# Optimization experiments

Measured on AMD Instinct MI355X. Metric: run time of the kernel, lower is better.

Reference implementation:

```python
import jax, jax.numpy as jnp
import numpy as np

B, NR, M, NL = 1, 384, 4, 128
IN_C, MID_C, OUT_C = 384, 32, 128


def setup_inputs() -> dict:
    key = jax.random.key(0)
    ks = jax.random.split(key, 24)
    s = 0.02
    d = {
        'rec_1d': jax.random.normal(ks[0], (B, NR, IN_C), jnp.float32),
        'lig_1d': jax.random.normal(ks[1], (B, M, NL, IN_C), jnp.float32),
        'pw_rep': jax.random.normal(ks[2], (B, NR + NL, NR + NL, OUT_C), jnp.float32),
        'rl1_w': jax.random.normal(ks[3], (MID_C, IN_C), jnp.float32) * s,
        'rl1_b': jax.random.normal(ks[4], (MID_C,), jnp.float32) * s,
        'rl2_w': jax.random.normal(ks[5], (MID_C, IN_C), jnp.float32) * s,
        'rl2_b': jax.random.normal(ks[6], (MID_C,), jnp.float32) * s,
        'll1_w': jax.random.normal(ks[7], (MID_C, IN_C), jnp.float32) * s,
        'll1_b': jax.random.normal(ks[8], (MID_C,), jnp.float32) * s,
        'll2_w': jax.random.normal(ks[9], (MID_C, IN_C), jnp.float32) * s,
        'll2_b': jax.random.normal(ks[10], (MID_C,), jnp.float32) * s,
        'rr_w': jax.random.normal(ks[11], (OUT_C, MID_C * MID_C), jnp.float32) * s,
        'rr_b': jax.random.normal(ks[12], (OUT_C,), jnp.float32) * s,
        'rl_w': jax.random.normal(ks[13], (OUT_C, MID_C * MID_C), jnp.float32) * s,
        'rl_b': jax.random.normal(ks[14], (OUT_C,), jnp.float32) * s,
        'lr_w': jax.random.normal(ks[15], (OUT_C, MID_C * MID_C), jnp.float32) * s,
        'lr_b': jax.random.normal(ks[16], (OUT_C,), jnp.float32) * s,
        'll_w': jax.random.normal(ks[17], (OUT_C, MID_C * MID_C), jnp.float32) * s,
        'll_b': jax.random.normal(ks[18], (OUT_C,), jnp.float32) * s,
    }
    return d


def reference(rec_1d, lig_1d, pw_rep,
              rl1_w, rl1_b, rl2_w, rl2_b,
              ll1_w, ll1_b, ll2_w, ll2_b,
              rr_w, rr_b, rl_w, rl_b, lr_w, lr_b, ll_w, ll_b):
    mid_c = rl1_w.shape[0]
    m = lig_1d.shape[1]

    # 1D projections (nn.Linear: x @ W.T + b)
    r_i = rec_1d @ rl1_w.T + rl1_b          # [b, NR, mid]
    r_j = rec_1d @ rl2_w.T + rl2_b          # [b, NR, mid]
    l_i = lig_1d @ ll1_w.T + ll1_b          # [b, m, NL, mid]
    l_j = lig_1d @ ll2_w.T + ll2_b          # [b, m, NL, mid]

    # final Linear weights over flattened (x, y) -> [out, x, y] (y fastest, matching .view)
    Wrr = rr_w.reshape(-1, mid_c, mid_c)
    Wrl = rl_w.reshape(-1, mid_c, mid_c)
    Wlr = lr_w.reshape(-1, mid_c, mid_c)
    Wll = ll_w.reshape(-1, mid_c, mid_c)

    # rr[b,i,j,o] = sum_xy r_i[b,i,x] r_j[b,j,y] Wrr[o,x,y]
    # contract projection weight with one factor first (OpenFold trick):
    rr = jnp.einsum('bioy,bjy->bijo', jnp.einsum('bix,oxy->bioy', r_i, Wrr), r_j) + rr_b

    # mean over m commutes with the broadcast outer products for rl/lr
    l_j_mean = l_j.mean(axis=1)             # [b, NL, mid]
    l_i_mean = l_i.mean(axis=1)             # [b, NL, mid]

    rl = jnp.einsum('bioy,bjy->bijo', jnp.einsum('bix,oxy->bioy', r_i, Wrl), l_j_mean) + rl_b

    # lr output is [b, j_lig, i_res, o]: x-axis from r_j, y-axis from l_i
    lr = jnp.einsum('bioy,bjy->bjio', jnp.einsum('bix,oxy->bioy', r_j, Wlr), l_i_mean) + lr_b

    # ll: mean over m of per-copy outer products (not separable)
    ll = jnp.einsum('bmioy,bmjy->bijo', jnp.einsum('bmix,oxy->bmioy', l_i, Wll), l_j) / m + ll_b

    top = jnp.concatenate([rr, rl], axis=2)  # [b, NR, NR+NL, out]
    bot = jnp.concatenate([lr, ll], axis=2)  # [b, NL, NR+NL, out]
    pw_update = jnp.concatenate([top, bot], axis=1).astype(pw_rep.dtype)
    return pw_update
```

## Files before the change

kernel.cpp:

```cpp
#include <hip/hip_runtime.h>

#define NRES 384
#define NLIG 128
#define INC 384
#define OUTC 128
#define NTOT 512

#define WS_RI   0
#define WS_RJ   12288
#define WS_LI   24576
#define WS_LJ   40960
#define WS_BF16 57344

#define BT_RR   0
#define BT_RL   1572864
#define BT_LR   3145728
#define BT_LL   4718592
#define BF_RJ   6815744
#define BF_LJM  6828032
#define BF_LIM  6832128
#define BF_LJ   6836224
#define BF_RI   6852608
#define BF_LI   6864896
#define BW_W    6881280

typedef __bf16 bf16x8 __attribute__((ext_vector_type(8)));
typedef __bf16 bf16x4 __attribute__((ext_vector_type(4)));
typedef float  f32x4  __attribute__((ext_vector_type(4)));

__device__ inline bf16x8 cvt8(const float* p) {
  f32x4 a = *(const f32x4*)p, b = *(const f32x4*)(p + 4);
  bf16x8 r;
  r[0] = (__bf16)a[0]; r[1] = (__bf16)a[1]; r[2] = (__bf16)a[2]; r[3] = (__bf16)a[3];
  r[4] = (__bf16)b[0]; r[5] = (__bf16)b[1]; r[6] = (__bf16)b[2]; r[7] = (__bf16)b[3];
  return r;
}

__global__ __launch_bounds__(256) void kP_proj(
    const float* __restrict__ rec, const float* __restrict__ lig,
    const float* __restrict__ rl1w, const float* __restrict__ rl1b,
    const float* __restrict__ rl2w, const float* __restrict__ rl2b,
    const float* __restrict__ ll1w, const float* __restrict__ ll1b,
    const float* __restrict__ ll2w, const float* __restrict__ ll2b,
    const float* __restrict__ Wrr, const float* __restrict__ Wrl,
    const float* __restrict__ Wlr, const float* __restrict__ Wll,
    float* __restrict__ ws) {
  __shared__ float lds[32 * 33];
  int b = blockIdx.x, t = threadIdx.x;
  __bf16* B16 = (__bf16*)(ws + WS_BF16);
  if (b >= 28) {
    int bb = b - 28;
    int tt = bb >> 7, o = bb & 127;
    const float* W = tt == 0 ? Wrr : tt == 1 ? Wrl : tt == 2 ? Wlr : Wll;
    __bf16* Wb = B16 + BW_W + tt * 131072;
#pragma unroll
    for (int k = 0; k < 4; ++k) {
      int idx = k * 256 + t;
      int x = idx >> 5, y = idx & 31;
      lds[y * 33 + x] = W[(size_t)o * 1024 + idx];
    }
    __syncthreads();
#pragma unroll
    for (int k = 0; k < 4; ++k) {
      int idx = k * 256 + t;
      int y = idx >> 5, x = idx & 31;
      Wb[(size_t)(o * 32 + y) * 32 + x] = (__bf16)lds[y * 33 + x];
    }
    return;
  }
  int l = t & 63, w = t >> 6;
  int lr16 = l & 15, lq = l >> 4;
  int pair = w >> 1, rh = w & 1;

  const float* in;
  const float *w1, *b1, *w2, *b2;
  float *o1, *o2;
  __bf16 *bf1, *bf2;
  int row0;
  if (b < 12) {
    row0 = b * 32;
    in = rec; w1 = rl1w; b1 = rl1b; w2 = rl2w; b2 = rl2b;
    o1 = ws + WS_RI; o2 = ws + WS_RJ;
    bf1 = B16 + BF_RI; bf2 = B16 + BF_RJ;
  } else {
    row0 = (b - 12) * 32;
    in = lig; w1 = ll1w; b1 = ll1b; w2 = ll2w; b2 = ll2b;
    o1 = ws + WS_LI; o2 = ws + WS_LJ;
    bf1 = B16 + BF_LI; bf2 = B16 + BF_LJ;
  }
  const float* wsrc = pair ? w2 : w1;
  const float* bsrc = pair ? b2 : b1;
  float* osrc = pair ? o2 : o1;
  __bf16* bdst = pair ? bf2 : bf1;
  int arow = row0 + rh * 16 + lr16;

  f32x4 acc[2];
#pragma unroll
  for (int ci = 0; ci < 2; ++ci) acc[ci] = (f32x4){0.f, 0.f, 0.f, 0.f};
  for (int ks = 0; ks < 12; ++ks) {
    bf16x8 af = cvt8(in + (size_t)arow * INC + ks * 32 + lq * 8);
#pragma unroll
    for (int ci = 0; ci < 2; ++ci) {
      int ch = ci * 16 + lr16;
      bf16x8 bf = cvt8(wsrc + (size_t)ch * INC + ks * 32 + lq * 8);
      acc[ci] = __builtin_amdgcn_mfma_f32_16x16x32_bf16(af, bf, acc[ci], 0, 0, 0);
    }
  }
#pragma unroll
  for (int ci = 0; ci < 2; ++ci) {
    int c = ci * 16 + lr16;
    float bias = bsrc[c];
#pragma unroll
    for (int e = 0; e < 4; ++e) {
      int r = row0 + rh * 16 + 4 * lq + e;
      float v = acc[ci][e] + bias;
      osrc[r * 32 + c] = v;
      bdst[r * 32 + c] = (__bf16)v;
    }
  }
}

#define TSTR 264
__global__ __launch_bounds__(256) void k2_makeA(float* __restrict__ ws) {
  __shared__ __bf16 tile[128 * TSTR];
  int b = blockIdx.x, t = threadIdx.x;
  __bf16* B16 = (__bf16*)(ws + WS_BF16);
  if (b >= 256) {
    const float* lj = ws + WS_LJ;
    const float* li = ws + WS_LI;
    __bf16* dm = B16 + BF_LJM;
    __bf16* di = B16 + BF_LIM;
    for (int k = 0; k < 16; ++k) {
      int idx = k * 256 + t;
      dm[idx] = (__bf16)(0.25f * (lj[idx] + lj[4096 + idx] + lj[8192 + idx] + lj[12288 + idx]));
      di[idx] = (__bf16)(0.25f * (li[idx] + li[4096 + idx] + li[8192 + idx] + li[12288 + idx]));
    }
    return;
  }
  int tt = b >> 6, sub = b & 63;
  int nt = sub >> 2, mq = sub & 3;
  const __bf16* facB;
  __bf16* At;
  int M;
  if (tt == 0)      { facB = B16 + BF_RI; At = B16 + BT_RR; M = 384; }
  else if (tt == 1) { facB = B16 + BF_RI; At = B16 + BT_RL; M = 384; }
  else if (tt == 2) { facB = B16 + BF_RJ; At = B16 + BT_LR; M = 384; }
  else              { facB = B16 + BF_LI; At = B16 + BT_LL; M = 512; }
  const __bf16* Wb = B16 + BW_W + tt * 131072;
  int l = t & 63, w = t >> 6;
  int lr16 = l & 15, lq = l >> 4;
  int nw = w * 64;
  int n0w = nt * 256 + nw;
  int mspan = M >> 2;
  int mtiles = M >> 6;
  int m0 = mq * mspan;

  bf16x8 wv[4];
#pragma unroll
  for (int q = 0; q < 4; ++q)
    wv[q] = *(const bf16x8*)(Wb + (size_t)(n0w + q * 16 + lr16) * 32 + lq * 8);

  for (int mt = 0; mt < mtiles; ++mt) {
    bf16x8 fv = *(const bf16x8*)(facB + (size_t)(m0 + mt * 16 + lr16) * 32 + lq * 8);
    f32x4 acc[4];
#pragma unroll
    for (int q = 0; q < 4; ++q) acc[q] = (f32x4){0.f, 0.f, 0.f, 0.f};
#pragma unroll
    for (int q = 0; q < 4; ++q)
      acc[q] = __builtin_amdgcn_mfma_f32_16x16x32_bf16(wv[q], fv, acc[q], 0, 0, 0);
    int ml = mt * 16 + lr16;
#pragma unroll
    for (int q = 0; q < 4; ++q) {
      bf16x4 v;
#pragma unroll
      for (int e = 0; e < 4; ++e) v[e] = (__bf16)acc[q][e];
      *(bf16x4*)&tile[ml * TSTR + nw + q * 16 + 4 * lq] = v;
    }
  }
  __syncthreads();
  int total8 = mspan * 32;
  for (int idx = t; idx < total8; idx += 256) {
    int m = idx >> 5, nl = (idx & 31) * 8;
    bf16x8 v = *(const bf16x8*)&tile[m * TSTR + nl];
    *(bf16x8*)(At + (size_t)(m0 + m) * 4096 + nt * 256 + nl) = v;
  }
}

__global__ __launch_bounds__(256) void k3_mfma(
    const float* __restrict__ ws, float* __restrict__ out,
    const float* __restrict__ rrb, const float* __restrict__ rlb,
    const float* __restrict__ lrb, const float* __restrict__ llb) {
  const __bf16* B16 = (const __bf16*)(ws + WS_BF16);
  int b = blockIdx.x, t = threadIdx.x;
  int l = t & 63, w = t >> 6;
  int lr16 = l & 15, lq = l >> 4;

  if (b < 1920) {
    const __bf16* At;
    const __bf16* fc;
    const float* bias;
    float* outp;
    size_t jstr;
    if (b < 1152) {
      int i = b / 3, jt = b - 3 * i;
      At = B16 + BT_RR + (size_t)i * 4096;
      fc = B16 + BF_RJ + jt * 4096;
      bias = rrb; outp = out + ((size_t)i * NTOT + jt * 128) * OUTC; jstr = OUTC;
    } else if (b < 1536) {
      int i = b - 1152;
      At = B16 + BT_RL + (size_t)i * 4096;
      fc = B16 + BF_LJM;
      bias = rlb; outp = out + ((size_t)i * NTOT + NRES) * OUTC; jstr = OUTC;
    } else {
      int i = b - 1536;
      At = B16 + BT_LR + (size_t)i * 4096;
      fc = B16 + BF_LIM;
      bias = lrb; outp = out + (size_t)NRES * NTOT * OUTC + (size_t)i * OUTC;
      jstr = (size_t)NTOT * OUTC;
    }
    bf16x8 fj[2];
#pragma unroll
    for (int jj = 0; jj < 2; ++jj)
      fj[jj] = *(const bf16x8*)(fc + (size_t)(w * 32 + jj * 16 + lr16) * 32 + lq * 8);
    f32x4 acc[2][8];
#pragma unroll
    for (int jj = 0; jj < 2; ++jj)
#pragma unroll
      for (int ot = 0; ot < 8; ++ot) acc[jj][ot] = (f32x4){0.f, 0.f, 0.f, 0.f};
#pragma unroll
    for (int oc = 0; oc < 2; ++oc) {
      bf16x8 av[4];
#pragma unroll
      for (int o4 = 0; o4 < 4; ++o4)
        av[o4] = *(const bf16x8*)(At + (size_t)((oc * 4 + o4) * 16 + lr16) * 32 + lq * 8);
#pragma unroll
      for (int jj = 0; jj < 2; ++jj)
#pragma unroll
        for (int o4 = 0; o4 < 4; ++o4)
          acc[jj][oc * 4 + o4] =
              __builtin_amdgcn_mfma_f32_16x16x32_bf16(av[o4], fj[jj], acc[jj][oc * 4 + o4], 0, 0, 0);
    }
#pragma unroll
    for (int jj = 0; jj < 2; ++jj) {
      int j = w * 32 + jj * 16 + lr16;
#pragma unroll
      for (int ot = 0; ot < 8; ++ot) {
        f32x4 b4 = *(const f32x4*)&bias[ot * 16 + 4 * lq];
        f32x4 v = acc[jj][ot] + b4;
        *(f32x4*)&outp[(size_t)j * jstr + ot * 16 + 4 * lq] = v;
      }
    }
  } else {
    int il = b - 1920;
    f32x4 acc[2][8];
#pragma unroll
    for (int jj = 0; jj < 2; ++jj)
#pragma unroll
      for (int ot = 0; ot < 8; ++ot) acc[jj][ot] = (f32x4){0.f, 0.f, 0.f, 0.f};
    for (int m = 0; m < 4; ++m) {
      const __bf16* At = B16 + BT_LL + (size_t)(m * 128 + il) * 4096;
      const __bf16* fc = B16 + BF_LJ + m * 4096;
      bf16x8 fj[2];
#pragma unroll
      for (int jj = 0; jj < 2; ++jj)
        fj[jj] = *(const bf16x8*)(fc + (size_t)(w * 32 + jj * 16 + lr16) * 32 + lq * 8);
#pragma unroll
      for (int oc = 0; oc < 2; ++oc) {
        bf16x8 av[4];
#pragma unroll
        for (int o4 = 0; o4 < 4; ++o4)
          av[o4] = *(const bf16x8*)(At + (size_t)((oc * 4 + o4) * 16 + lr16) * 32 + lq * 8);
#pragma unroll
        for (int jj = 0; jj < 2; ++jj)
#pragma unroll
          for (int o4 = 0; o4 < 4; ++o4)
            acc[jj][oc * 4 + o4] =
                __builtin_amdgcn_mfma_f32_16x16x32_bf16(av[o4], fj[jj], acc[jj][oc * 4 + o4], 0, 0, 0);
      }
    }
    float* outp = out + ((size_t)(NRES + il) * NTOT + NRES) * OUTC;
#pragma unroll
    for (int jj = 0; jj < 2; ++jj) {
      int j = w * 32 + jj * 16 + lr16;
#pragma unroll
      for (int ot = 0; ot < 8; ++ot) {
        f32x4 b4 = *(const f32x4*)&llb[ot * 16 + 4 * lq];
        f32x4 v = 0.25f * acc[jj][ot] + b4;
        *(f32x4*)&outp[(size_t)j * OUTC + ot * 16 + 4 * lq] = v;
      }
    }
  }
}

extern "C" void kernel_launch(void* const* d_in, const int* in_sizes, int n_in,
                              void* d_out, int out_size, void* d_ws, size_t ws_size,
                              hipStream_t stream) {
  const float* rec  = (const float*)d_in[0];
  const float* lig  = (const float*)d_in[1];
  const float* rl1w = (const float*)d_in[3];
  const float* rl1b = (const float*)d_in[4];
  const float* rl2w = (const float*)d_in[5];
  const float* rl2b = (const float*)d_in[6];
  const float* ll1w = (const float*)d_in[7];
  const float* ll1b = (const float*)d_in[8];
  const float* ll2w = (const float*)d_in[9];
  const float* ll2b = (const float*)d_in[10];
  const float* rrw  = (const float*)d_in[11];
  const float* rrb  = (const float*)d_in[12];
  const float* rlw  = (const float*)d_in[13];
  const float* rlb  = (const float*)d_in[14];
  const float* lrw  = (const float*)d_in[15];
  const float* lrb  = (const float*)d_in[16];
  const float* llw  = (const float*)d_in[17];
  const float* llb  = (const float*)d_in[18];
  float* out = (float*)d_out;
  float* ws  = (float*)d_ws;

  hipLaunchKernelGGL(kP_proj, dim3(540), dim3(256), 0, stream,
                     rec, lig, rl1w, rl1b, rl2w, rl2b, ll1w, ll1b, ll2w, ll2b,
                     rrw, rlw, lrw, llw, ws);
  hipLaunchKernelGGL(k2_makeA, dim3(257), dim3(256), 0, stream, ws);
  hipLaunchKernelGGL(k3_mfma, dim3(2048), dim3(256), 0, stream,
                     ws, out, rrb, rlb, lrb, llb);
}
```

Baseline: 50.79 us.

## Fuse projection and A-matrix build into one kernel, compute ligand means in consumer

```diff
diff --git a/kernel.cpp b/kernel.cpp
--- a/kernel.cpp
+++ b/kernel.cpp
@@ -6,23 +6,17 @@
 #define OUTC 128
 #define NTOT 512
 
-#define WS_RI   0
-#define WS_RJ   12288
-#define WS_LI   24576
-#define WS_LJ   40960
-#define WS_BF16 57344
-
 #define BT_RR   0
 #define BT_RL   1572864
 #define BT_LR   3145728
 #define BT_LL   4718592
 #define BF_RJ   6815744
-#define BF_LJM  6828032
-#define BF_LIM  6832128
-#define BF_LJ   6836224
-#define BF_RI   6852608
-#define BF_LI   6864896
-#define BW_W    6881280
+#define BF_LJ   6828032
+#define BF_LI   6844416
+
+#define FSTR 40
+#define WSTR 40
+#define TSTR 264
 
 typedef __bf16 bf16x8 __attribute__((ext_vector_type(8)));
 typedef __bf16 bf16x4 __attribute__((ext_vector_type(4)));
@@ -36,7 +30,7 @@
   return r;
 }
 
-__global__ __launch_bounds__(256) void kP_proj(
+__global__ __launch_bounds__(256) void kA_make(
     const float* __restrict__ rec, const float* __restrict__ lig,
     const float* __restrict__ rl1w, const float* __restrict__ rl1b,
     const float* __restrict__ rl2w, const float* __restrict__ rl2b,
@@ -45,144 +39,115 @@
     const float* __restrict__ Wrr, const float* __restrict__ Wrl,
     const float* __restrict__ Wlr, const float* __restrict__ Wll,
     float* __restrict__ ws) {
-  __shared__ float lds[32 * 33];
+  __shared__ __align__(16) char arena[77824];
+  __bf16* wb    = (__bf16*)arena;
+  __bf16* tileO = (__bf16*)arena;
+  __bf16* facB  = (__bf16*)(arena + 67584);
+  __bf16* B16 = (__bf16*)ws;
   int b = blockIdx.x, t = threadIdx.x;
-  __bf16* B16 = (__bf16*)(ws + WS_BF16);
-  if (b >= 28) {
-    int bb = b - 28;
-    int tt = bb >> 7, o = bb & 127;
-    const float* W = tt == 0 ? Wrr : tt == 1 ? Wrl : tt == 2 ? Wlr : Wll;
-    __bf16* Wb = B16 + BW_W + tt * 131072;
-#pragma unroll
-    for (int k = 0; k < 4; ++k) {
-      int idx = k * 256 + t;
-      int x = idx >> 5, y = idx & 31;
-      lds[y * 33 + x] = W[(size_t)o * 1024 + idx];
-    }
-    __syncthreads();
-#pragma unroll
-    for (int k = 0; k < 4; ++k) {
-      int idx = k * 256 + t;
-      int y = idx >> 5, x = idx & 31;
-      Wb[(size_t)(o * 32 + y) * 32 + x] = (__bf16)lds[y * 33 + x];
-    }
-    return;
-  }
   int l = t & 63, w = t >> 6;
   int lr16 = l & 15, lq = l >> 4;
-  int pair = w >> 1, rh = w & 1;
-
-  const float* in;
-  const float *w1, *b1, *w2, *b2;
-  float *o1, *o2;
-  __bf16 *bf1, *bf2;
-  int row0;
-  if (b < 12) {
-    row0 = b * 32;
-    in = rec; w1 = rl1w; b1 = rl1b; w2 = rl2w; b2 = rl2b;
-    o1 = ws + WS_RI; o2 = ws + WS_RJ;
-    bf1 = B16 + BF_RI; bf2 = B16 + BF_RJ;
+
+  if (b < 256) {
+    int tt = b >> 6, sub = b & 63;
+    int nt = sub >> 2, mq = sub & 3;
+    const float *in, *w1, *b1, *W;
+    __bf16* AtG;
+    int mspan;
+    if (tt == 0)      { in = rec; w1 = rl1w; b1 = rl1b; W = Wrr; AtG = B16 + BT_RR; mspan = 96; }
+    else if (tt == 1) { in = rec; w1 = rl1w; b1 = rl1b; W = Wrl; AtG = B16 + BT_RL; mspan = 96; }
+    else if (tt == 2) { in = rec; w1 = rl2w; b1 = rl2b; W = Wlr; AtG = B16 + BT_LR; mspan = 96; }
+    else              { in = lig; w1 = ll1w; b1 = ll1b; W = Wll; AtG = B16 + BT_LL; mspan = 128; }
+    int m0 = mq * mspan, o0 = nt * 8;
+
+#pragma unroll
+    for (int it = 0; it < 8; ++it) {
+      int idx4 = it * 256 + t;
+      f32x4 v = *(const f32x4*)(W + (size_t)o0 * 1024 + idx4 * 4);
+      int flat = idx4 * 4;
+      int oo = flat >> 10, r = flat & 1023, x = r >> 5, y0 = r & 31;
+#pragma unroll
+      for (int e = 0; e < 4; ++e)
+        wb[(oo * 32 + y0 + e) * WSTR + x] = (__bf16)v[e];
+    }
+    __syncthreads();
+
+    bf16x8 wv[4];
+    int nw = w * 64;
+#pragma unroll
+    for (int q = 0; q < 4; ++q)
+      wv[q] = *(const bf16x8*)&wb[(nw + q * 16 + lr16) * WSTR + lq * 8];
+
+    int rtiles = mspan >> 4;
+    int tpw = (rtiles * 2) >> 2;
+    for (int ti = 0; ti < tpw; ++ti) {
+      int tile = w * tpw + ti;
+      int rt = tile >> 1, ct = tile & 1;
+      int ch = ct * 16 + lr16;
+      int arow = m0 + rt * 16 + lr16;
+      f32x4 acc = (f32x4){0.f, 0.f, 0.f, 0.f};
+      for (int ks = 0; ks < 12; ++ks) {
+        bf16x8 af = cvt8(in + (size_t)arow * INC + ks * 32 + lq * 8);
+        bf16x8 bf = cvt8(w1 + (size_t)ch * INC + ks * 32 + lq * 8);
+        acc = __builtin_amdgcn_mfma_f32_16x16x32_bf16(af, bf, acc, 0, 0, 0);
+      }
+      float bias = b1[ch];
+#pragma unroll
+      for (int e = 0; e < 4; ++e)
+        facB[(rt * 16 + 4 * lq + e) * FSTR + ch] = (__bf16)(acc[e] + bias);
+    }
+    __syncthreads();
+
+    for (int mt = 0; mt < rtiles; ++mt) {
+      bf16x8 fv = *(const bf16x8*)&facB[(mt * 16 + lr16) * FSTR + lq * 8];
+      f32x4 acc[4];
+#pragma unroll
+      for (int q = 0; q < 4; ++q) acc[q] = (f32x4){0.f, 0.f, 0.f, 0.f};
+#pragma unroll
+      for (int q = 0; q < 4; ++q)
+        acc[q] = __builtin_amdgcn_mfma_f32_16x16x32_bf16(wv[q], fv, acc[q], 0, 0, 0);
+      int ml = mt * 16 + lr16;
+#pragma unroll
+      for (int q = 0; q < 4; ++q) {
+        bf16x4 v;
+#pragma unroll
+        for (int e = 0; e < 4; ++e) v[e] = (__bf16)acc[q][e];
+        *(bf16x4*)&tileO[ml * TSTR + nw + q * 16 + 4 * lq] = v;
+      }
+    }
+    __syncthreads();
+    int total8 = mspan * 32;
+    for (int idx = t; idx < total8; idx += 256) {
+      int m = idx >> 5, nl = (idx & 31) * 8;
+      bf16x8 v = *(const bf16x8*)&tileO[m * TSTR + nl];
+      *(bf16x8*)(AtG + (size_t)(m0 + m) * 4096 + nt * 256 + nl) = v;
+    }
   } else {
-    row0 = (b - 12) * 32;
-    in = lig; w1 = ll1w; b1 = ll1b; w2 = ll2w; b2 = ll2b;
-    o1 = ws + WS_LI; o2 = ws + WS_LJ;
-    bf1 = B16 + BF_LI; bf2 = B16 + BF_LJ;
-  }
-  const float* wsrc = pair ? w2 : w1;
-  const float* bsrc = pair ? b2 : b1;
-  float* osrc = pair ? o2 : o1;
-  __bf16* bdst = pair ? bf2 : bf1;
-  int arow = row0 + rh * 16 + lr16;
-
-  f32x4 acc[2];
-#pragma unroll
-  for (int ci = 0; ci < 2; ++ci) acc[ci] = (f32x4){0.f, 0.f, 0.f, 0.f};
-  for (int ks = 0; ks < 12; ++ks) {
-    bf16x8 af = cvt8(in + (size_t)arow * INC + ks * 32 + lq * 8);
-#pragma unroll
-    for (int ci = 0; ci < 2; ++ci) {
-      int ch = ci * 16 + lr16;
-      bf16x8 bf = cvt8(wsrc + (size_t)ch * INC + ks * 32 + lq * 8);
-      acc[ci] = __builtin_amdgcn_mfma_f32_16x16x32_bf16(af, bf, acc[ci], 0, 0, 0);
-    }
-  }
-#pragma unroll
-  for (int ci = 0; ci < 2; ++ci) {
-    int c = ci * 16 + lr16;
-    float bias = bsrc[c];
-#pragma unroll
-    for (int e = 0; e < 4; ++e) {
-      int r = row0 + rh * 16 + 4 * lq + e;
-      float v = acc[ci][e] + bias;
-      osrc[r * 32 + c] = v;
-      bdst[r * 32 + c] = (__bf16)v;
-    }
-  }
-}
-
-#define TSTR 264
-__global__ __launch_bounds__(256) void k2_makeA(float* __restrict__ ws) {
-  __shared__ __bf16 tile[128 * TSTR];
-  int b = blockIdx.x, t = threadIdx.x;
-  __bf16* B16 = (__bf16*)(ws + WS_BF16);
-  if (b >= 256) {
-    const float* lj = ws + WS_LJ;
-    const float* li = ws + WS_LI;
-    __bf16* dm = B16 + BF_LJM;
-    __bf16* di = B16 + BF_LIM;
-    for (int k = 0; k < 16; ++k) {
-      int idx = k * 256 + t;
-      dm[idx] = (__bf16)(0.25f * (lj[idx] + lj[4096 + idx] + lj[8192 + idx] + lj[12288 + idx]));
-      di[idx] = (__bf16)(0.25f * (li[idx] + li[4096 + idx] + li[8192 + idx] + li[12288 + idx]));
-    }
-    return;
-  }
-  int tt = b >> 6, sub = b & 63;
-  int nt = sub >> 2, mq = sub & 3;
-  const __bf16* facB;
-  __bf16* At;
-  int M;
-  if (tt == 0)      { facB = B16 + BF_RI; At = B16 + BT_RR; M = 384; }
-  else if (tt == 1) { facB = B16 + BF_RI; At = B16 + BT_RL; M = 384; }
-  else if (tt == 2) { facB = B16 + BF_RJ; At = B16 + BT_LR; M = 384; }
-  else              { facB = B16 + BF_LI; At = B16 + BT_LL; M = 512; }
-  const __bf16* Wb = B16 + BW_W + tt * 131072;
-  int l = t & 63, w = t >> 6;
-  int lr16 = l & 15, lq = l >> 4;
-  int nw = w * 64;
-  int n0w = nt * 256 + nw;
-  int mspan = M >> 2;
-  int mtiles = M >> 6;
-  int m0 = mq * mspan;
-
-  bf16x8 wv[4];
-#pragma unroll
-  for (int q = 0; q < 4; ++q)
-    wv[q] = *(const bf16x8*)(Wb + (size_t)(n0w + q * 16 + lr16) * 32 + lq * 8);
-
-  for (int mt = 0; mt < mtiles; ++mt) {
-    bf16x8 fv = *(const bf16x8*)(facB + (size_t)(m0 + mt * 16 + lr16) * 32 + lq * 8);
-    f32x4 acc[4];
-#pragma unroll
-    for (int q = 0; q < 4; ++q) acc[q] = (f32x4){0.f, 0.f, 0.f, 0.f};
-#pragma unroll
-    for (int q = 0; q < 4; ++q)
-      acc[q] = __builtin_amdgcn_mfma_f32_16x16x32_bf16(wv[q], fv, acc[q], 0, 0, 0);
-    int ml = mt * 16 + lr16;
-#pragma unroll
-    for (int q = 0; q < 4; ++q) {
-      bf16x4 v;
-#pragma unroll
-      for (int e = 0; e < 4; ++e) v[e] = (__bf16)acc[q][e];
-      *(bf16x4*)&tile[ml * TSTR + nw + q * 16 + 4 * lq] = v;
-    }
-  }
-  __syncthreads();
-  int total8 = mspan * 32;
-  for (int idx = t; idx < total8; idx += 256) {
-    int m = idx >> 5, nl = (idx & 31) * 8;
-    bf16x8 v = *(const bf16x8*)&tile[m * TSTR + nl];
-    *(bf16x8*)(At + (size_t)(m0 + m) * 4096 + nt * 256 + nl) = v;
+    int tb = b - 256;
+    const float *in, *wsrc, *bsrc;
+    __bf16* outb;
+    int rows, row0;
+    if (tb < 2)      { in = rec; wsrc = rl2w; bsrc = rl2b; outb = B16 + BF_RJ; rows = 192; row0 = tb * 192; }
+    else if (tb < 4) { in = lig; wsrc = ll2w; bsrc = ll2b; outb = B16 + BF_LJ; rows = 256; row0 = (tb - 2) * 256; }
+    else             { in = lig; wsrc = ll1w; bsrc = ll1b; outb = B16 + BF_LI; rows = 256; row0 = (tb - 4) * 256; }
+    int rtiles = rows >> 4;
+    int tpw = (rtiles * 2) >> 2;
+    for (int ti = 0; ti < tpw; ++ti) {
+      int tile = w * tpw + ti;
+      int rt = tile >> 1, ct = tile & 1;
+      int ch = ct * 16 + lr16;
+      int arow = row0 + rt * 16 + lr16;
+      f32x4 acc = (f32x4){0.f, 0.f, 0.f, 0.f};
+      for (int ks = 0; ks < 12; ++ks) {
+        bf16x8 af = cvt8(in + (size_t)arow * INC + ks * 32 + lq * 8);
+        bf16x8 bf = cvt8(wsrc + (size_t)ch * INC + ks * 32 + lq * 8);
+        acc = __builtin_amdgcn_mfma_f32_16x16x32_bf16(af, bf, acc, 0, 0, 0);
+      }
+      float bias = bsrc[ch];
+#pragma unroll
+      for (int e = 0; e < 4; ++e)
+        outb[(size_t)(row0 + rt * 16 + 4 * lq + e) * 32 + ch] = (__bf16)(acc[e] + bias);
+    }
   }
 }
 
@@ -190,38 +155,63 @@
     const float* __restrict__ ws, float* __restrict__ out,
     const float* __restrict__ rrb, const float* __restrict__ rlb,
     const float* __restrict__ lrb, const float* __restrict__ llb) {
-  const __bf16* B16 = (const __bf16*)(ws + WS_BF16);
+  const __bf16* B16 = (const __bf16*)ws;
   int b = blockIdx.x, t = threadIdx.x;
   int l = t & 63, w = t >> 6;
   int lr16 = l & 15, lq = l >> 4;
 
   if (b < 1920) {
     const __bf16* At;
-    const __bf16* fc;
     const float* bias;
     float* outp;
     size_t jstr;
+    bf16x8 fj[2];
     if (b < 1152) {
       int i = b / 3, jt = b - 3 * i;
       At = B16 + BT_RR + (size_t)i * 4096;
-      fc = B16 + BF_RJ + jt * 4096;
+      const __bf16* fc = B16 + BF_RJ + jt * 4096;
+#pragma unroll
+      for (int jj = 0; jj < 2; ++jj)
+        fj[jj] = *(const bf16x8*)(fc + (size_t)(w * 32 + jj * 16 + lr16) * 32 + lq * 8);
       bias = rrb; outp = out + ((size_t)i * NTOT + jt * 128) * OUTC; jstr = OUTC;
     } else if (b < 1536) {
       int i = b - 1152;
       At = B16 + BT_RL + (size_t)i * 4096;
-      fc = B16 + BF_LJM;
+      const __bf16* lj = B16 + BF_LJ;
+#pragma unroll
+      for (int jj = 0; jj < 2; ++jj) {
+        size_t off = (size_t)(w * 32 + jj * 16 + lr16) * 32 + lq * 8;
+        float s[8] = {0, 0, 0, 0, 0, 0, 0, 0};
+#pragma unroll
+        for (int mm = 0; mm < 4; ++mm) {
+          bf16x8 v = *(const bf16x8*)(lj + mm * 4096 + off);
+#pragma unroll
+          for (int e = 0; e < 8; ++e) s[e] += (float)v[e];
+        }
+#pragma unroll
+        for (int e = 0; e < 8; ++e) fj[jj][e] = (__bf16)(0.25f * s[e]);
+      }
       bias = rlb; outp = out + ((size_t)i * NTOT + NRES) * OUTC; jstr = OUTC;
     } else {
       int i = b - 1536;
       At = B16 + BT_LR + (size_t)i * 4096;
-      fc = B16 + BF_LIM;
+      const __bf16* li = B16 + BF_LI;
+#pragma unroll
+      for (int jj = 0; jj < 2; ++jj) {
+        size_t off = (size_t)(w * 32 + jj * 16 + lr16) * 32 + lq * 8;
+        float s[8] = {0, 0, 0, 0, 0, 0, 0, 0};
+#pragma unroll
+        for (int mm = 0; mm < 4; ++mm) {
+          bf16x8 v = *(const bf16x8*)(li + mm * 4096 + off);
+#pragma unroll
+          for (int e = 0; e < 8; ++e) s[e] += (float)v[e];
+        }
+#pragma unroll
+        for (int e = 0; e < 8; ++e) fj[jj][e] = (__bf16)(0.25f * s[e]);
+      }
       bias = lrb; outp = out + (size_t)NRES * NTOT * OUTC + (size_t)i * OUTC;
       jstr = (size_t)NTOT * OUTC;
     }
-    bf16x8 fj[2];
-#pragma unroll
-    for (int jj = 0; jj < 2; ++jj)
-      fj[jj] = *(const bf16x8*)(fc + (size_t)(w * 32 + jj * 16 + lr16) * 32 + lq * 8);
     f32x4 acc[2][8];
 #pragma unroll
     for (int jj = 0; jj < 2; ++jj)
@@ -316,10 +306,9 @@
   float* out = (float*)d_out;
   float* ws  = (float*)d_ws;
 
-  hipLaunchKernelGGL(kP_proj, dim3(540), dim3(256), 0, stream,
+  hipLaunchKernelGGL(kA_make, dim3(262), dim3(256), 0, stream,
                      rec, lig, rl1w, rl1b, rl2w, rl2b, ll1w, ll1b, ll2w, ll2b,
                      rrw, rlw, lrw, llw, ws);
-  hipLaunchKernelGGL(k2_makeA, dim3(257), dim3(256), 0, stream, ws);
   hipLaunchKernelGGL(k3_mfma, dim3(2048), dim3(256), 0, stream,
                      ws, out, rrb, rlb, lrb, llb);
 }
```

Result: slower. 93.60 us (+84.3%).
